# Performance work log

Measured on AMD Instinct MI355X. Metric: run time of the kernel, lower is better.

The kernel has to match this reference:

```python
import jax, jax.numpy as jnp
import numpy as np

DIM = 1024
NUM_HEADS = 16
HEAD_DIM = DIM // NUM_HEADS
SCALE = HEAD_DIM ** -0.5
HIDDEN = int(DIM * 1.0)


def setup_inputs() -> dict:
    key = jax.random.key(0)
    ks = jax.random.split(key, 11)
    s = 0.02
    return {
        "x":  jax.random.normal(ks[0], (2, 2048, DIM), jnp.float32),
        "Wq": jax.random.normal(ks[1], (DIM, DIM), jnp.float32) * s,
        "bq": jnp.zeros((DIM,), jnp.float32),
        "Wk": jax.random.normal(ks[2], (DIM, DIM), jnp.float32) * s,
        "bk": jnp.zeros((DIM,), jnp.float32),
        "Wv": jax.random.normal(ks[3], (DIM, DIM), jnp.float32) * s,
        "bv": jnp.zeros((DIM,), jnp.float32),
        "W1": jax.random.normal(ks[4], (HIDDEN, DIM), jnp.float32) * s,
        "b1": jnp.zeros((HIDDEN,), jnp.float32),
        "W2": jax.random.normal(ks[5], (DIM, HIDDEN), jnp.float32) * s,
        "b2": jnp.zeros((DIM,), jnp.float32),
    }


def _split_heads(t, B, S):
    # [B,S,C] -> [B,H,S,hd]
    return t.reshape(B, S, NUM_HEADS, HEAD_DIM).transpose(0, 2, 1, 3)


def reference(x, Wq, bq, Wk, bk, Wv, bv, W1, b1, W2, b2):
    B, S, C = x.shape
    q = _split_heads(x @ Wq.T + bq, B, S) * SCALE
    k = _split_heads(x @ Wk.T + bk, B, S)
    v = _split_heads(x @ Wv.T + bv, B, S)
    # softmax-free bilinear attention, scores in float32 (matches .float())
    attn = jnp.einsum('bhqd,bhkd->bhqk', q.astype(jnp.float32), k.astype(jnp.float32))
    out = jnp.einsum('bhqk,bhkd->bhqd', attn, v)  # [B,H,S,hd]
    out = out.transpose(0, 2, 1, 3).reshape(B, S, C)
    h = jax.nn.gelu(out @ W1.T + b1, approximate=False)
    mlp = h @ W2.T + b2
    return x + out + mlp
```

## Files before the change

kernel.cpp:

```cpp
#include <hip/hip_runtime.h>
#include <math.h>

#define DIM    1024
#define BATCH  2
#define SEQ    2048
#define NHEAD  16
#define HDIM   64
#define MROWS  (BATCH*SEQ)
#define NSPLIT 8

typedef unsigned short u16;
typedef __attribute__((ext_vector_type(8))) short  s16x8;
typedef __attribute__((ext_vector_type(4))) float  f32x4;

typedef __attribute__((address_space(3))) unsigned int       lds_u32_t;
typedef const __attribute__((address_space(1))) unsigned int glb_u32_t;

__device__ __forceinline__ float bf2f(u16 h) {
    unsigned u = ((unsigned)h) << 16; float f; __builtin_memcpy(&f, &u, 4); return f;
}
__device__ __forceinline__ u16 f2bf(float f) {
    unsigned u; __builtin_memcpy(&u, &f, 4);
    u += 0x7FFFu + ((u >> 16) & 1u);
    return (u16)(u >> 16);
}

__global__ __launch_bounds__(256)
void pack_all(const float* __restrict__ x,
              const float* __restrict__ Wq, const float* __restrict__ Wk,
              const float* __restrict__ Wv, const float* __restrict__ W1,
              const float* __restrict__ W2,
              u16* __restrict__ xb, u16* __restrict__ Wqb, u16* __restrict__ Wkb,
              u16* __restrict__ Wvb, u16* __restrict__ W1b, u16* __restrict__ W2b)
{
    const int bid = blockIdx.x;
    const float* src; u16* dst; int i;
    if (bid < 4096) { src = x; dst = xb; i = bid * 256 + threadIdx.x; }
    else {
        const int w = (bid - 4096) >> 10;
        const int lb = (bid - 4096) & 1023;
        src = (w == 0) ? Wq : (w == 1) ? Wk : (w == 2) ? Wv : (w == 3) ? W1 : W2;
        dst = (w == 0) ? Wqb : (w == 1) ? Wkb : (w == 2) ? Wvb : (w == 3) ? W1b : W2b;
        i = lb * 256 + threadIdx.x;
    }
    float4 v = ((const float4*)src)[i];
    ushort4 o = { f2bf(v.x), f2bf(v.y), f2bf(v.z), f2bf(v.w) };
    ((ushort4*)dst)[i] = o;
}

__device__ __forceinline__ void stage_tile(const u16* __restrict__ gbase, int k0,
                                           u16* lds, int tid)
{
    #pragma unroll
    for (int p = 0; p < 2; ++p) {
        int e   = p * 256 + tid;
        int row = e >> 2;
        int cg  = e & 3;
        const u16* src = gbase + (size_t)row * DIM + k0 + cg * 8;
        __builtin_amdgcn_global_load_lds((glb_u32_t*)src, (lds_u32_t*)(lds + e * 8), 16, 0, 0);
    }
}

__device__ __forceinline__ void gemm_core_m97(const u16* __restrict__ Ab,
                                              const u16* __restrict__ Bb,
                                              u16* As, u16* Bs, int tid,
                                              f32x4 acc[4][4])
{
    const int w = tid >> 6, l = tid & 63;
    const int wm = (w >> 1) * 64, wn = (w & 1) * 64;
    const int lr = l & 15, kq = l >> 4;

    for (int k0 = 0; k0 < DIM; k0 += 32) {
        stage_tile(Ab, k0, As, tid);
        stage_tile(Bb, k0, Bs, tid);
        __syncthreads();
        s16x8 af[4], bfr[4];
        #pragma unroll
        for (int i = 0; i < 4; ++i)
            af[i]  = *(const s16x8*)(As + (wm + i * 16 + lr) * 32 + kq * 8);
        #pragma unroll
        for (int j = 0; j < 4; ++j)
            bfr[j] = *(const s16x8*)(Bs + (wn + j * 16 + lr) * 32 + kq * 8);
        #pragma unroll
        for (int i = 0; i < 4; ++i)
            #pragma unroll
            for (int j = 0; j < 4; ++j)
                acc[i][j] = __builtin_amdgcn_mfma_f32_16x16x32_bf16(af[i], bfr[j], acc[i][j], 0, 0, 0);
        __syncthreads();
    }
}

__device__ __forceinline__ void gemm_core4_m64(const u16* __restrict__ Ab,
                                               const u16* __restrict__ Bb,
                                               u16* As , u16* Bs ,
                                               int tid, f32x4 acc[2][4])
{
    const int w  = tid >> 6, l = tid & 63;
    const int wm = (w >> 1) * 32, wn = (w & 1) * 64;
    const int lr = l & 15, kq = l >> 4;
    const int ar = tid >> 2, acg = tid & 3;

    for (int k0 = 0; k0 < DIM; k0 += 32) {
        const u16* srcA = Ab + (size_t)ar * DIM + k0 + acg * 8;
        __builtin_amdgcn_global_load_lds((glb_u32_t*)srcA, (lds_u32_t*)(As + tid * 8), 16, 0, 0);
        #pragma unroll
        for (int j = 0; j < 2; ++j) {
            const int cid = j * 256 + tid;
            const int br = cid >> 2, bcg = cid & 3;
            const u16* srcB = Bb + (size_t)br * DIM + k0 + bcg * 8;
            __builtin_amdgcn_global_load_lds((glb_u32_t*)srcB, (lds_u32_t*)(Bs + cid * 8), 16, 0, 0);
        }
        __syncthreads();
        s16x8 af[2], bfr[4];
        #pragma unroll
        for (int i = 0; i < 2; ++i)
            af[i]  = *(const s16x8*)(As + (wm + i * 16 + lr) * 32 + kq * 8);
        #pragma unroll
        for (int j = 0; j < 4; ++j)
            bfr[j] = *(const s16x8*)(Bs + (wn + j * 16 + lr) * 32 + kq * 8);
        #pragma unroll
        for (int i = 0; i < 2; ++i)
            #pragma unroll
            for (int j = 0; j < 4; ++j)
                acc[i][j] = __builtin_amdgcn_mfma_f32_16x16x32_bf16(af[i], bfr[j], acc[i][j], 0, 0, 0);
        __syncthreads();
    }
}

__global__ __launch_bounds__(256)
void qkv_gemm(const u16* __restrict__ xb,
              const u16* __restrict__ Wq, const u16* __restrict__ Wk, const u16* __restrict__ Wv,
              const float* __restrict__ bq, const float* __restrict__ bk, const float* __restrict__ bv,
              u16* __restrict__ qo, u16* __restrict__ ko, u16* __restrict__ vo)
{
    __shared__ u16 As[128 * 32];
    __shared__ u16 Bs[128 * 32];
    const int tid = threadIdx.x;
    const int m0  = blockIdx.x * 128;
    const int sel = blockIdx.y >> 3;
    const int n0  = (blockIdx.y & 7) * 128;
    const u16*   B    = (sel == 0) ? Wq : (sel == 1) ? Wk : Wv;
    const float* bias = (sel == 0) ? bq : (sel == 1) ? bk : bv;
    u16*         C    = (sel == 0) ? qo : (sel == 1) ? ko : vo;
    const float scale = (sel == 0) ? 0.125f : 1.0f;

    f32x4 acc[4][4];
    #pragma unroll
    for (int i = 0; i < 4; ++i)
        #pragma unroll
        for (int j = 0; j < 4; ++j) acc[i][j] = (f32x4){0.f, 0.f, 0.f, 0.f};

    gemm_core_m97(xb + (size_t)m0 * DIM, B + (size_t)n0 * DIM, As, Bs, tid, acc);

    const int w = tid >> 6, l = tid & 63;
    const int wm = (w >> 1) * 64, wn = (w & 1) * 64;
    const int er = l >> 4, ec = l & 15;
    #pragma unroll
    for (int j = 0; j < 4; ++j) {
        const int n = n0 + wn + j * 16 + ec;
        const float bb = bias[n];
        #pragma unroll
        for (int i = 0; i < 4; ++i)
            #pragma unroll
            for (int r = 0; r < 4; ++r) {
                const int m = m0 + wm + i * 16 + er * 4 + r;
                C[(size_t)m * DIM + n] = f2bf((acc[i][j][r] + bb) * scale);
            }
    }
}

__global__ __launch_bounds__(256)
void gemm_bf16(const u16* __restrict__ A, const u16* __restrict__ B,
               const float* __restrict__ bias,
               u16* __restrict__ Cb, float* __restrict__ Cf,
               const float* __restrict__ rx, const u16* __restrict__ rattn,
               int mode)
{
    __shared__ u16 As[64 * 32];
    __shared__ u16 Bs[128 * 32];
    const int tid = threadIdx.x;
    const int m0 = blockIdx.x * 64, n0 = blockIdx.y * 128;

    f32x4 acc[2][4];
    #pragma unroll
    for (int i = 0; i < 2; ++i)
        #pragma unroll
        for (int j = 0; j < 4; ++j) acc[i][j] = (f32x4){0.f, 0.f, 0.f, 0.f};

    gemm_core4_m64(A + (size_t)m0 * DIM, B + (size_t)n0 * DIM, As, Bs, tid, acc);

    const int w = tid >> 6, l = tid & 63;
    const int wm = (w >> 1) * 32, wn = (w & 1) * 64;
    const int er = l >> 4, ec = l & 15;
    #pragma unroll
    for (int j = 0; j < 4; ++j) {
        const int n = n0 + wn + j * 16 + ec;
        const float bb = bias[n];
        #pragma unroll
        for (int i = 0; i < 2; ++i)
            #pragma unroll
            for (int r = 0; r < 4; ++r) {
                const int m = m0 + wm + i * 16 + er * 4 + r;
                const size_t idx = (size_t)m * DIM + n;
                float v = acc[i][j][r] + bb;
                if (mode == 1) {
                    v = 0.5f * v * (1.0f + erff(v * 0.70710678118654752f));
                    Cb[idx] = f2bf(v);
                } else {
                    Cf[idx] = v + rx[idx] + bf2f(rattn[idx]);
                }
            }
    }
}

__global__ __launch_bounds__(256)
void ktv_mfma(const u16* __restrict__ Kb, const u16* __restrict__ Vb,
              float* __restrict__ part)
{
    __shared__ u16 Kt[64 * 264];
    __shared__ u16 Vt[64 * 264];
    const int tid = threadIdx.x;
    const int bh = blockIdx.x & 31;
    const int sp = blockIdx.x >> 5;
    const int b = bh >> 4, h = bh & 15;
    const size_t base = (size_t)b * SEQ * DIM + (size_t)h * HDIM + (size_t)sp * 256 * DIM;

    const int dg = (tid & 15) * 4;
    #pragma unroll
    for (int pass = 0; pass < 16; ++pass) {
        const int s = (tid >> 4) + 16 * pass;
        ushort4 kv = *(const ushort4*)(Kb + base + (size_t)s * DIM + dg);
        ushort4 vv = *(const ushort4*)(Vb + base + (size_t)s * DIM + dg);
        Kt[(dg + 0) * 264 + s] = kv.x; Kt[(dg + 1) * 264 + s] = kv.y;
        Kt[(dg + 2) * 264 + s] = kv.z; Kt[(dg + 3) * 264 + s] = kv.w;
        Vt[(dg + 0) * 264 + s] = vv.x; Vt[(dg + 1) * 264 + s] = vv.y;
        Vt[(dg + 2) * 264 + s] = vv.z; Vt[(dg + 3) * 264 + s] = vv.w;
    }
    __syncthreads();

    const int w = tid >> 6, l = tid & 63;
    const int lr = l & 15, kq = l >> 4;
    f32x4 acc[4];
    #pragma unroll
    for (int j = 0; j < 4; ++j) acc[j] = (f32x4){0.f, 0.f, 0.f, 0.f};

    for (int k0 = 0; k0 < 256; k0 += 32) {
        s16x8 af = *(const s16x8*)(Kt + (w * 16 + lr) * 264 + k0 + kq * 8);
        #pragma unroll
        for (int j = 0; j < 4; ++j) {
            s16x8 bf = *(const s16x8*)(Vt + (j * 16 + lr) * 264 + k0 + kq * 8);
            acc[j] = __builtin_amdgcn_mfma_f32_16x16x32_bf16(af, bf, acc[j], 0, 0, 0);
        }
    }

    float* dst = part + ((size_t)sp * 32 + bh) * (HDIM * HDIM);
    const int er = l >> 4, ec = l & 15;
    #pragma unroll
    for (int j = 0; j < 4; ++j)
        #pragma unroll
        for (int r = 0; r < 4; ++r)
            dst[(w * 16 + er * 4 + r) * HDIM + j * 16 + ec] = acc[j][r];
}

__global__ __launch_bounds__(256)
void qktv_kernel(const u16* __restrict__ Qb, const float* __restrict__ part,
                 u16* __restrict__ attnb)
{
    __shared__ float KV[HDIM * HDIM];
    __shared__ u16 Qs[128 * 68];
    const int tid = threadIdx.x;
    const int h  = blockIdx.x;
    const int mt = blockIdx.y;
    const int row0 = mt * 128;
    const int b = row0 >> 11;
    const int bh = b * NHEAD + h;

    for (int i = tid; i < HDIM * HDIM; i += 256) {
        float s = 0.f;
        #pragma unroll
        for (int sp = 0; sp < NSPLIT; ++sp)
            s += part[((size_t)sp * 32 + bh) * (HDIM * HDIM) + i];
        KV[i] = s;
    }
    const int dg = (tid & 15) * 4;
    #pragma unroll
    for (int pass = 0; pass < 8; ++pass) {
        const int r = (tid >> 4) + 16 * pass;
        ushort4 q = *(const ushort4*)(Qb + (size_t)(row0 + r) * DIM + h * HDIM + dg);
        *(ushort4*)(Qs + r * 68 + dg) = q;
    }
    __syncthreads();

    const int tr = tid >> 3, tc = tid & 7;
    const int r0 = tr * 4, c0 = tc * 8;
    float acc[4][8] = {};
    for (int d = 0; d < HDIM; ++d) {
        float4 ka  = *(const float4*)&KV[d * HDIM + c0];
        float4 kb2 = *(const float4*)&KV[d * HDIM + c0 + 4];
        const float* k8a = (const float*)&ka;
        const float* k8b = (const float*)&kb2;
        float qv[4];
        #pragma unroll
        for (int i = 0; i < 4; ++i) qv[i] = bf2f(Qs[(r0 + i) * 68 + d]);
        #pragma unroll
        for (int i = 0; i < 4; ++i)
            #pragma unroll
            for (int j = 0; j < 4; ++j) {
                acc[i][j]     += qv[i] * k8a[j];
                acc[i][j + 4] += qv[i] * k8b[j];
            }
    }
    #pragma unroll
    for (int i = 0; i < 4; ++i) {
        u16* dst = attnb + (size_t)(row0 + r0 + i) * DIM + h * HDIM + c0;
        ushort4 o0 = { f2bf(acc[i][0]), f2bf(acc[i][1]), f2bf(acc[i][2]), f2bf(acc[i][3]) };
        ushort4 o1 = { f2bf(acc[i][4]), f2bf(acc[i][5]), f2bf(acc[i][6]), f2bf(acc[i][7]) };
        *(ushort4*)(dst)     = o0;
        *(ushort4*)(dst + 4) = o1;
    }
}

extern "C" void kernel_launch(void* const* d_in, const int* in_sizes, int n_in,
                              void* d_out, int out_size, void* d_ws, size_t ws_size,
                              hipStream_t stream)
{
    const float* x  = (const float*)d_in[0];
    const float* Wq = (const float*)d_in[1];
    const float* bq = (const float*)d_in[2];
    const float* Wk = (const float*)d_in[3];
    const float* bk = (const float*)d_in[4];
    const float* Wv = (const float*)d_in[5];
    const float* bv = (const float*)d_in[6];
    const float* W1 = (const float*)d_in[7];
    const float* b1 = (const float*)d_in[8];
    const float* W2 = (const float*)d_in[9];
    const float* b2 = (const float*)d_in[10];
    float* out = (float*)d_out;

    char* ws = (char*)d_ws;
    const size_t MB = 1u << 20;
    u16* xb   = (u16*)(ws);
    u16* Wqb  = (u16*)(ws +  8 * MB);
    u16* Wkb  = (u16*)(ws + 10 * MB);
    u16* Wvb  = (u16*)(ws + 12 * MB);
    u16* W1b  = (u16*)(ws + 14 * MB);
    u16* W2b  = (u16*)(ws + 16 * MB);
    u16* qb   = (u16*)(ws + 18 * MB);
    u16* kb   = (u16*)(ws + 26 * MB);
    u16* vb   = (u16*)(ws + 34 * MB);
    float* part = (float*)(ws + 42 * MB);
    u16* attnb = kb;
    u16* h1b   = vb;

    pack_all<<<4096 + 5 * 1024, 256, 0, stream>>>(x, Wq, Wk, Wv, W1, W2,
                                                  xb, Wqb, Wkb, Wvb, W1b, W2b);

    qkv_gemm<<<dim3(32, 24), 256, 0, stream>>>(xb, Wqb, Wkb, Wvb, bq, bk, bv, qb, kb, vb);

    ktv_mfma<<<NSPLIT * 32, 256, 0, stream>>>(kb, vb, part);
    qktv_kernel<<<dim3(NHEAD, MROWS / 128), 256, 0, stream>>>(qb, part, attnb);

    gemm_bf16<<<dim3(64, 8), 256, 0, stream>>>(attnb, W1b, b1, h1b, nullptr, nullptr, nullptr, 1);
    gemm_bf16<<<dim3(64, 8), 256, 0, stream>>>(h1b, W2b, b2, nullptr, out, x, attnb, 2);
}
```

Measured before the change: 203.9 us.

## Double-buffer GEMM LDS tiles with register prefetch instead of direct global-to-LDS loads

Both GEMM cores (QKV and the generic 64-row GEMM) stop using global_load_lds with two barriers per k-step. They now load the next k-slice into registers while the MFMAs run on the current LDS buffer, then write it into a second LDS buffer, which leaves one barrier per iteration. This is meant to hide global memory latency behind compute and halve synchronisation. In exchange it doubles LDS use, adds VGPR pressure, and adds an extra register-to-LDS store pass.

```diff
diff --git a/kernel.cpp b/kernel.cpp
--- a/kernel.cpp
+++ b/kernel.cpp
@@ -12,9 +12,6 @@
 typedef unsigned short u16;
 typedef __attribute__((ext_vector_type(8))) short  s16x8;
 typedef __attribute__((ext_vector_type(4))) float  f32x4;
-
-typedef __attribute__((address_space(3))) unsigned int       lds_u32_t;
-typedef const __attribute__((address_space(1))) unsigned int glb_u32_t;
 
 __device__ __forceinline__ float bf2f(u16 h) {
     unsigned u = ((unsigned)h) << 16; float f; __builtin_memcpy(&f, &u, 4); return f;
@@ -48,49 +45,58 @@
     ((ushort4*)dst)[i] = o;
 }
 
-__device__ __forceinline__ void stage_tile(const u16* __restrict__ gbase, int k0,
-                                           u16* lds, int tid)
-{
-    #pragma unroll
-    for (int p = 0; p < 2; ++p) {
-        int e   = p * 256 + tid;
-        int row = e >> 2;
-        int cg  = e & 3;
-        const u16* src = gbase + (size_t)row * DIM + k0 + cg * 8;
-        __builtin_amdgcn_global_load_lds((glb_u32_t*)src, (lds_u32_t*)(lds + e * 8), 16, 0, 0);
-    }
-}
-
-__device__ __forceinline__ void gemm_core_m97(const u16* __restrict__ Ab,
-                                              const u16* __restrict__ Bb,
-                                              u16* As, u16* Bs, int tid,
-                                              f32x4 acc[4][4])
+__device__ __forceinline__ void gemm_core_pf128(const u16* __restrict__ Ab,
+                                                const u16* __restrict__ Bb,
+                                                u16* As, u16* Bs,
+                                                int tid, f32x4 acc[4][4])
 {
     const int w = tid >> 6, l = tid & 63;
     const int wm = (w >> 1) * 64, wn = (w & 1) * 64;
     const int lr = l & 15, kq = l >> 4;
-
-    for (int k0 = 0; k0 < DIM; k0 += 32) {
-        stage_tile(Ab, k0, As, tid);
-        stage_tile(Bb, k0, Bs, tid);
+    const int row = tid >> 2, cg8 = (tid & 3) * 8;
+
+    const u16* a0 = Ab + (size_t)row * DIM + cg8;
+    const u16* a1 = Ab + (size_t)(64 + row) * DIM + cg8;
+    const u16* b0 = Bb + (size_t)row * DIM + cg8;
+    const u16* b1 = Bb + (size_t)(64 + row) * DIM + cg8;
+
+    uint4 pa0 = *(const uint4*)a0, pa1 = *(const uint4*)a1;
+    uint4 pb0 = *(const uint4*)b0, pb1 = *(const uint4*)b1;
+    *(uint4*)(As + tid * 8) = pa0;  *(uint4*)(As + 2048 + tid * 8) = pa1;
+    *(uint4*)(Bs + tid * 8) = pb0;  *(uint4*)(Bs + 2048 + tid * 8) = pb1;
+
+    const int NIT = DIM / 32;
+    for (int it = 0; it < NIT; ++it) {
+        u16* Ac = As + (it & 1) * 4096;
+        u16* Bc = Bs + (it & 1) * 4096;
         __syncthreads();
+        if (it + 1 < NIT) {
+            const int k = (it + 1) * 32;
+            pa0 = *(const uint4*)(a0 + k); pa1 = *(const uint4*)(a1 + k);
+            pb0 = *(const uint4*)(b0 + k); pb1 = *(const uint4*)(b1 + k);
+        }
         s16x8 af[4], bfr[4];
         #pragma unroll
         for (int i = 0; i < 4; ++i)
-            af[i]  = *(const s16x8*)(As + (wm + i * 16 + lr) * 32 + kq * 8);
+            af[i]  = *(const s16x8*)(Ac + (wm + i * 16 + lr) * 32 + kq * 8);
         #pragma unroll
         for (int j = 0; j < 4; ++j)
-            bfr[j] = *(const s16x8*)(Bs + (wn + j * 16 + lr) * 32 + kq * 8);
+            bfr[j] = *(const s16x8*)(Bc + (wn + j * 16 + lr) * 32 + kq * 8);
         #pragma unroll
         for (int i = 0; i < 4; ++i)
             #pragma unroll
             for (int j = 0; j < 4; ++j)
                 acc[i][j] = __builtin_amdgcn_mfma_f32_16x16x32_bf16(af[i], bfr[j], acc[i][j], 0, 0, 0);
-        __syncthreads();
-    }
-}
-
-__device__ __forceinline__ void gemm_core4_m64(const u16* __restrict__ Ab,
+        if (it + 1 < NIT) {
+            u16* An = As + ((it + 1) & 1) * 4096;
+            u16* Bn = Bs + ((it + 1) & 1) * 4096;
+            *(uint4*)(An + tid * 8) = pa0;  *(uint4*)(An + 2048 + tid * 8) = pa1;
+            *(uint4*)(Bn + tid * 8) = pb0;  *(uint4*)(Bn + 2048 + tid * 8) = pb1;
+        }
+    }
+}
+
+__device__ __forceinline__ void gemm_core_pf64(const u16* __restrict__ Ab,
                                                const u16* __restrict__ Bb,
                                                u16* As , u16* Bs ,
                                                int tid, f32x4 acc[2][4])
@@ -98,32 +104,45 @@
     const int w  = tid >> 6, l = tid & 63;
     const int wm = (w >> 1) * 32, wn = (w & 1) * 64;
     const int lr = l & 15, kq = l >> 4;
-    const int ar = tid >> 2, acg = tid & 3;
-
-    for (int k0 = 0; k0 < DIM; k0 += 32) {
-        const u16* srcA = Ab + (size_t)ar * DIM + k0 + acg * 8;
-        __builtin_amdgcn_global_load_lds((glb_u32_t*)srcA, (lds_u32_t*)(As + tid * 8), 16, 0, 0);
-        #pragma unroll
-        for (int j = 0; j < 2; ++j) {
-            const int cid = j * 256 + tid;
-            const int br = cid >> 2, bcg = cid & 3;
-            const u16* srcB = Bb + (size_t)br * DIM + k0 + bcg * 8;
-            __builtin_amdgcn_global_load_lds((glb_u32_t*)srcB, (lds_u32_t*)(Bs + cid * 8), 16, 0, 0);
-        }
+    const int row = tid >> 2, cg8 = (tid & 3) * 8;
+
+    const u16* a0 = Ab + (size_t)row * DIM + cg8;
+    const u16* b0 = Bb + (size_t)row * DIM + cg8;
+    const u16* b1 = Bb + (size_t)(64 + row) * DIM + cg8;
+
+    uint4 pa  = *(const uint4*)a0;
+    uint4 pb0 = *(const uint4*)b0, pb1 = *(const uint4*)b1;
+    *(uint4*)(As + tid * 8) = pa;
+    *(uint4*)(Bs + tid * 8) = pb0; *(uint4*)(Bs + 2048 + tid * 8) = pb1;
+
+    const int NIT = DIM / 32;
+    for (int it = 0; it < NIT; ++it) {
+        u16* Ac = As + (it & 1) * 2048;
+        u16* Bc = Bs + (it & 1) * 4096;
         __syncthreads();
+        if (it + 1 < NIT) {
+            const int k = (it + 1) * 32;
+            pa  = *(const uint4*)(a0 + k);
+            pb0 = *(const uint4*)(b0 + k); pb1 = *(const uint4*)(b1 + k);
+        }
         s16x8 af[2], bfr[4];
         #pragma unroll
         for (int i = 0; i < 2; ++i)
-            af[i]  = *(const s16x8*)(As + (wm + i * 16 + lr) * 32 + kq * 8);
+            af[i]  = *(const s16x8*)(Ac + (wm + i * 16 + lr) * 32 + kq * 8);
         #pragma unroll
         for (int j = 0; j < 4; ++j)
-            bfr[j] = *(const s16x8*)(Bs + (wn + j * 16 + lr) * 32 + kq * 8);
+            bfr[j] = *(const s16x8*)(Bc + (wn + j * 16 + lr) * 32 + kq * 8);
         #pragma unroll
         for (int i = 0; i < 2; ++i)
             #pragma unroll
             for (int j = 0; j < 4; ++j)
                 acc[i][j] = __builtin_amdgcn_mfma_f32_16x16x32_bf16(af[i], bfr[j], acc[i][j], 0, 0, 0);
-        __syncthreads();
+        if (it + 1 < NIT) {
+            u16* An = As + ((it + 1) & 1) * 2048;
+            u16* Bn = Bs + ((it + 1) & 1) * 4096;
+            *(uint4*)(An + tid * 8) = pa;
+            *(uint4*)(Bn + tid * 8) = pb0; *(uint4*)(Bn + 2048 + tid * 8) = pb1;
+        }
     }
 }
 
@@ -133,8 +152,8 @@
               const float* __restrict__ bq, const float* __restrict__ bk, const float* __restrict__ bv,
               u16* __restrict__ qo, u16* __restrict__ ko, u16* __restrict__ vo)
 {
-    __shared__ u16 As[128 * 32];
-    __shared__ u16 Bs[128 * 32];
+    __shared__ u16 As[2 * 4096];
+    __shared__ u16 Bs[2 * 4096];
     const int tid = threadIdx.x;
     const int m0  = blockIdx.x * 128;
     const int sel = blockIdx.y >> 3;
@@ -150,7 +169,7 @@
         #pragma unroll
         for (int j = 0; j < 4; ++j) acc[i][j] = (f32x4){0.f, 0.f, 0.f, 0.f};
 
-    gemm_core_m97(xb + (size_t)m0 * DIM, B + (size_t)n0 * DIM, As, Bs, tid, acc);
+    gemm_core_pf128(xb + (size_t)m0 * DIM, B + (size_t)n0 * DIM, As, Bs, tid, acc);
 
     const int w = tid >> 6, l = tid & 63;
     const int wm = (w >> 1) * 64, wn = (w & 1) * 64;
@@ -176,8 +195,8 @@
                const float* __restrict__ rx, const u16* __restrict__ rattn,
                int mode)
 {
-    __shared__ u16 As[64 * 32];
-    __shared__ u16 Bs[128 * 32];
+    __shared__ u16 As[2 * 2048];
+    __shared__ u16 Bs[2 * 4096];
     const int tid = threadIdx.x;
     const int m0 = blockIdx.x * 64, n0 = blockIdx.y * 128;
 
@@ -187,7 +206,7 @@
         #pragma unroll
         for (int j = 0; j < 4; ++j) acc[i][j] = (f32x4){0.f, 0.f, 0.f, 0.f};
 
-    gemm_core4_m64(A + (size_t)m0 * DIM, B + (size_t)n0 * DIM, As, Bs, tid, acc);
+    gemm_core_pf64(A + (size_t)m0 * DIM, B + (size_t)n0 * DIM, As, Bs, tid, acc);
 
     const int w = tid >> 6, l = tid & 63;
     const int wm = (w >> 1) * 32, wn = (w & 1) * 64;
```

After: 203.7 us. Within noise of the previous version (-0.1%).
